# Optimization experiments

Measured on AMD Instinct MI355X. Metric: run time of the kernel, lower is better.

Reference implementation:

```python
import jax, jax.numpy as jnp
import numpy as np

E, T, H, I = 16, 512, 1024, 4096


def setup_inputs() -> dict:
    key = jax.random.key(0)
    k_x, k_w1, k_b1, k_w2, k_b2 = jax.random.split(key, 5)
    scale = 0.02
    return {
        "route_results": jax.random.normal(k_x, (E, T, H), dtype=jnp.float32),
        "W1": jax.random.normal(k_w1, (E, H, I), dtype=jnp.float32) * scale,
        "b1": jax.random.normal(k_b1, (E, I), dtype=jnp.float32) * scale,
        "W2": jax.random.normal(k_w2, (E, I, H), dtype=jnp.float32) * scale,
        "b2": jax.random.normal(k_b2, (E, H), dtype=jnp.float32) * scale,
    }


def reference(route_results, W1, b1, W2, b2):
    # Per-expert 2-layer linear MLP (no activation in source), expressed as
    # a single grouped (batched) GEMM over the expert axis e.
    h = jnp.einsum("eth,ehi->eti", route_results, W1) + b1[:, None, :]
    y = jnp.einsum("eti,eih->eth", h, W2) + b2[:, None, :]
    # torch.cat(expert_results, dim=0): stack expert outputs along token dim.
    e, t, hid = y.shape
    return y.reshape(e * t, hid)
```

## Files before the change

### kernel.cpp

```cpp
#include <hip/hip_runtime.h>
#include <stdint.h>


#define E_ 16
#define T_ 512
#define H_ 1024
#define I_ 4096

typedef _Float16 f16x8 __attribute__((ext_vector_type(8)));
typedef __fp16   h2    __attribute__((ext_vector_type(2)));
typedef float    f32x4 __attribute__((ext_vector_type(4)));

#define LDK 40

template <bool A_IS_F16, bool OUT_IS_F16>
__global__ __launch_bounds__(256, 2) void moe_gemm(const void* __restrict__ Aall,
                                                   const float* __restrict__ Ball,
                                                   const float* __restrict__ biasAll,
                                                   void* __restrict__ Call,
                                                   int M, int N, int K) {
    __shared__ _Float16 sA[128 * LDK];
    __shared__ _Float16 sB[128 * LDK];

    const int e   = blockIdx.z;
    const int m0  = blockIdx.y * 128;
    const int n0  = blockIdx.x * 128;
    const int tid = threadIdx.x;
    const int lane = tid & 63;
    const int wave = tid >> 6;
    const int wm = (wave >> 1) * 64;
    const int wn = (wave & 1) * 64;
    const int lrow = lane & 15;
    const int lk8  = (lane >> 4) * 8;

    const float* B_e    = Ball + (size_t)e * K * N;
    const float* bias_e = biasAll + (size_t)e * N;
    const float*     A_f32 = (const float*)Aall + (size_t)e * M * K;
    const _Float16*  A_f16 = (const _Float16*)Aall + (size_t)e * M * K;

    const int bn  = ((tid >> 6) & 1) * 64 + (tid & 63);
    const int bkh = (tid >> 7) * 16;
    const int ar = (tid >> 6) * 32 + ((tid & 63) >> 2);
    const int ak = (tid & 3) * 8;

    f32x4 acc[4][4];
    const f32x4 zero = {0.f, 0.f, 0.f, 0.f};
#pragma unroll
    for (int i = 0; i < 4; ++i)
#pragma unroll
        for (int j = 0; j < 4; ++j) acc[i][j] = zero;

    for (int k0 = 0; k0 < K; k0 += 32) {
        if (A_IS_F16) {
            const int r  = tid >> 2;
            const int c8 = (tid & 3) * 8;
#pragma unroll
            for (int p = 0; p < 2; ++p) {
                const int row = r + p * 64;
                f16x8 v = *(const f16x8*)(A_f16 + (size_t)(m0 + row) * K + k0 + c8);
                *(f16x8*)&sA[row * LDK + c8] = v;
            }
        } else {
#pragma unroll
            for (int p = 0; p < 2; ++p) {
                const int row = ar + p * 16;
                const float* asrc = A_f32 + (size_t)(m0 + row) * K + k0 + ak;
                f32x4 va = *(const f32x4*)asrc;
                f32x4 vb = *(const f32x4*)(asrc + 4);
                f16x8 w;
                ((h2*)&w)[0] = __builtin_amdgcn_cvt_pkrtz(va.x, va.y);
                ((h2*)&w)[1] = __builtin_amdgcn_cvt_pkrtz(va.z, va.w);
                ((h2*)&w)[2] = __builtin_amdgcn_cvt_pkrtz(vb.x, vb.y);
                ((h2*)&w)[3] = __builtin_amdgcn_cvt_pkrtz(vb.z, vb.w);
                *(f16x8*)&sA[row * LDK + ak] = w;
            }
        }
        {
            const float* bsrc = B_e + (size_t)(k0 + bkh) * N + n0 + bn;
            float bv[16];
#pragma unroll
            for (int kk = 0; kk < 16; ++kk)
                bv[kk] = bsrc[(size_t)kk * N];
            f16x8 w0, w1;
#pragma unroll
            for (int j = 0; j < 4; ++j) {
                ((h2*)&w0)[j] = __builtin_amdgcn_cvt_pkrtz(bv[2 * j],     bv[2 * j + 1]);
                ((h2*)&w1)[j] = __builtin_amdgcn_cvt_pkrtz(bv[8 + 2 * j], bv[8 + 2 * j + 1]);
            }
            *(f16x8*)&sB[bn * LDK + bkh]     = w0;
            *(f16x8*)&sB[bn * LDK + bkh + 8] = w1;
        }
        __syncthreads();

        f16x8 af[4], bf[4];
#pragma unroll
        for (int mi = 0; mi < 4; ++mi)
            af[mi] = *(const f16x8*)&sA[(wm + mi * 16 + lrow) * LDK + lk8];
#pragma unroll
        for (int ni = 0; ni < 4; ++ni)
            bf[ni] = *(const f16x8*)&sB[(wn + ni * 16 + lrow) * LDK + lk8];
#pragma unroll
        for (int mi = 0; mi < 4; ++mi)
#pragma unroll
            for (int ni = 0; ni < 4; ++ni)
                acc[mi][ni] = __builtin_amdgcn_mfma_f32_16x16x32_f16(af[mi], bf[ni], acc[mi][ni], 0, 0, 0);
        __syncthreads();
    }

    const int row_base = (lane >> 4) * 4;
#pragma unroll
    for (int ni = 0; ni < 4; ++ni) {
        const int n = n0 + wn + ni * 16 + lrow;
        const float bv = bias_e[n];
#pragma unroll
        for (int mi = 0; mi < 4; ++mi) {
            const int mbase = m0 + wm + mi * 16 + row_base;
#pragma unroll
            for (int r = 0; r < 4; ++r) {
                const float val = acc[mi][ni][r] + bv;
                const size_t idx = (size_t)e * M * N + (size_t)(mbase + r) * N + n;
                if (OUT_IS_F16)
                    ((_Float16*)Call)[idx] = (_Float16)val;
                else
                    ((float*)Call)[idx] = val;
            }
        }
    }
}

extern "C" void kernel_launch(void* const* d_in, const int* in_sizes, int n_in,
                              void* d_out, int out_size, void* d_ws, size_t ws_size,
                              hipStream_t stream) {
    (void)in_sizes; (void)n_in; (void)out_size; (void)ws_size;
    const float* x  = (const float*)d_in[0];
    const float* W1 = (const float*)d_in[1];
    const float* b1 = (const float*)d_in[2];
    const float* W2 = (const float*)d_in[3];
    const float* b2 = (const float*)d_in[4];
    float* out = (float*)d_out;
    _Float16* hbuf = (_Float16*)d_ws;

    dim3 blk(256, 1, 1);
    dim3 g1(I_ / 128, T_ / 128, E_);
    moe_gemm<false, true><<<g1, blk, 0, stream>>>((const void*)x, W1, b1, (void*)hbuf, T_, I_, H_);
    dim3 g2(H_ / 128, T_ / 128, E_);
    moe_gemm<true, false><<<g2, blk, 0, stream>>>((const void*)hbuf, W2, b2, (void*)out, T_, H_, I_);
}
```

Before: 720.1 us.

## Prefetch next K-tile into registers while computing current tile

Splits each tile's global load from its LDS store and issues the load for the next K step before the MFMA work on the current one, so global memory latency overlaps with compute. The barrier placement changes to one barrier before the store and one after. This keeps extra live registers (16 floats for B plus the A values) across the MFMA loop, which may hurt occupancy under the 2-blocks-per-SM launch bound.

```diff
diff --git a/kernel.cpp b/kernel.cpp
--- a/kernel.cpp
+++ b/kernel.cpp
@@ -42,6 +42,55 @@
     const int bkh = (tid >> 7) * 16;
     const int ar = (tid >> 6) * 32 + ((tid & 63) >> 2);
     const int ak = (tid & 3) * 8;
+    const int r  = tid >> 2;
+    const int c8 = (tid & 3) * 8;
+
+    float bv[16];
+    f32x4 a32[4];
+    f16x8 a16[2];
+
+    auto load_tile = [&](int k0) {
+        const float* bsrc = B_e + (size_t)(k0 + bkh) * N + n0 + bn;
+#pragma unroll
+        for (int kk = 0; kk < 16; ++kk)
+            bv[kk] = bsrc[(size_t)kk * N];
+        if (A_IS_F16) {
+            a16[0] = *(const f16x8*)(A_f16 + (size_t)(m0 + r) * K + k0 + c8);
+            a16[1] = *(const f16x8*)(A_f16 + (size_t)(m0 + r + 64) * K + k0 + c8);
+        } else {
+            const float* a0 = A_f32 + (size_t)(m0 + ar) * K + k0 + ak;
+            a32[0] = *(const f32x4*)a0;
+            a32[1] = *(const f32x4*)(a0 + 4);
+            const float* a1 = A_f32 + (size_t)(m0 + ar + 16) * K + k0 + ak;
+            a32[2] = *(const f32x4*)a1;
+            a32[3] = *(const f32x4*)(a1 + 4);
+        }
+    };
+
+    auto store_tile = [&]() {
+        f16x8 w0, w1;
+#pragma unroll
+        for (int j = 0; j < 4; ++j) {
+            ((h2*)&w0)[j] = __builtin_amdgcn_cvt_pkrtz(bv[2 * j],     bv[2 * j + 1]);
+            ((h2*)&w1)[j] = __builtin_amdgcn_cvt_pkrtz(bv[8 + 2 * j], bv[8 + 2 * j + 1]);
+        }
+        *(f16x8*)&sB[bn * LDK + bkh]     = w0;
+        *(f16x8*)&sB[bn * LDK + bkh + 8] = w1;
+        if (A_IS_F16) {
+            *(f16x8*)&sA[r * LDK + c8]        = a16[0];
+            *(f16x8*)&sA[(r + 64) * LDK + c8] = a16[1];
+        } else {
+#pragma unroll
+            for (int p = 0; p < 2; ++p) {
+                f16x8 w;
+                ((h2*)&w)[0] = __builtin_amdgcn_cvt_pkrtz(a32[2 * p].x, a32[2 * p].y);
+                ((h2*)&w)[1] = __builtin_amdgcn_cvt_pkrtz(a32[2 * p].z, a32[2 * p].w);
+                ((h2*)&w)[2] = __builtin_amdgcn_cvt_pkrtz(a32[2 * p + 1].x, a32[2 * p + 1].y);
+                ((h2*)&w)[3] = __builtin_amdgcn_cvt_pkrtz(a32[2 * p + 1].z, a32[2 * p + 1].w);
+                *(f16x8*)&sA[(ar + p * 16) * LDK + ak] = w;
+            }
+        }
+    };
 
     f32x4 acc[4][4];
     const f32x4 zero = {0.f, 0.f, 0.f, 0.f};
@@ -50,46 +99,13 @@
 #pragma unroll
         for (int j = 0; j < 4; ++j) acc[i][j] = zero;
 
+    load_tile(0);
+
     for (int k0 = 0; k0 < K; k0 += 32) {
-        if (A_IS_F16) {
-            const int r  = tid >> 2;
-            const int c8 = (tid & 3) * 8;
-#pragma unroll
-            for (int p = 0; p < 2; ++p) {
-                const int row = r + p * 64;
-                f16x8 v = *(const f16x8*)(A_f16 + (size_t)(m0 + row) * K + k0 + c8);
-                *(f16x8*)&sA[row * LDK + c8] = v;
-            }
-        } else {
-#pragma unroll
-            for (int p = 0; p < 2; ++p) {
-                const int row = ar + p * 16;
-                const float* asrc = A_f32 + (size_t)(m0 + row) * K + k0 + ak;
-                f32x4 va = *(const f32x4*)asrc;
-                f32x4 vb = *(const f32x4*)(asrc + 4);
-                f16x8 w;
-                ((h2*)&w)[0] = __builtin_amdgcn_cvt_pkrtz(va.x, va.y);
-                ((h2*)&w)[1] = __builtin_amdgcn_cvt_pkrtz(va.z, va.w);
-                ((h2*)&w)[2] = __builtin_amdgcn_cvt_pkrtz(vb.x, vb.y);
-                ((h2*)&w)[3] = __builtin_amdgcn_cvt_pkrtz(vb.z, vb.w);
-                *(f16x8*)&sA[row * LDK + ak] = w;
-            }
-        }
-        {
-            const float* bsrc = B_e + (size_t)(k0 + bkh) * N + n0 + bn;
-            float bv[16];
-#pragma unroll
-            for (int kk = 0; kk < 16; ++kk)
-                bv[kk] = bsrc[(size_t)kk * N];
-            f16x8 w0, w1;
-#pragma unroll
-            for (int j = 0; j < 4; ++j) {
-                ((h2*)&w0)[j] = __builtin_amdgcn_cvt_pkrtz(bv[2 * j],     bv[2 * j + 1]);
-                ((h2*)&w1)[j] = __builtin_amdgcn_cvt_pkrtz(bv[8 + 2 * j], bv[8 + 2 * j + 1]);
-            }
-            *(f16x8*)&sB[bn * LDK + bkh]     = w0;
-            *(f16x8*)&sB[bn * LDK + bkh + 8] = w1;
-        }
+        __syncthreads();
+        store_tile();
+        if (k0 + 32 < K)
+            load_tile(k0 + 32);
         __syncthreads();
 
         f16x8 af[4], bf[4];
@@ -104,21 +120,20 @@
 #pragma unroll
             for (int ni = 0; ni < 4; ++ni)
                 acc[mi][ni] = __builtin_amdgcn_mfma_f32_16x16x32_f16(af[mi], bf[ni], acc[mi][ni], 0, 0, 0);
-        __syncthreads();
     }
 
     const int row_base = (lane >> 4) * 4;
 #pragma unroll
     for (int ni = 0; ni < 4; ++ni) {
         const int n = n0 + wn + ni * 16 + lrow;
-        const float bv = bias_e[n];
+        const float bv2 = bias_e[n];
 #pragma unroll
         for (int mi = 0; mi < 4; ++mi) {
             const int mbase = m0 + wm + mi * 16 + row_base;
 #pragma unroll
-            for (int r = 0; r < 4; ++r) {
-                const float val = acc[mi][ni][r] + bv;
-                const size_t idx = (size_t)e * M * N + (size_t)(mbase + r) * N + n;
+            for (int rr = 0; rr < 4; ++rr) {
+                const float val = acc[mi][ni][rr] + bv2;
+                const size_t idx = (size_t)e * M * N + (size_t)(mbase + rr) * N + n;
                 if (OUT_IS_F16)
                     ((_Float16*)Call)[idx] = (_Float16)val;
                 else
```

Result: faster. 705.9 us (-2.0%).
